# Kernel tuning notes

Hardware: AMD Instinct MI355X
Metric: run time of the kernel (lower is better)

## Reference

```python
import jax, jax.numpy as jnp
import numpy as np

B, L, D, H = 4, 2048, 1024, 16
DH = D // H


def setup_inputs() -> dict:
    key = jax.random.key(0)
    ks = jax.random.split(key, 8)
    scale = 1.0 / np.sqrt(D)
    q = jax.random.normal(ks[0], (B, L, D), dtype=jnp.float32)
    k = jax.random.normal(ks[1], (B, L, D), dtype=jnp.float32)
    v = jax.random.normal(ks[2], (B, L, D), dtype=jnp.float32)
    # causal mask: 1 = attend, 0 = masked (masked_fill(mask == 0, -inf))
    mask = jnp.tril(jnp.ones((L, L), dtype=bool))[None, None, :, :]
    mask = jnp.broadcast_to(mask, (B, 1, L, L))
    W_q = jax.random.normal(ks[3], (D, D), dtype=jnp.float32) * scale
    W_k = jax.random.normal(ks[4], (D, D), dtype=jnp.float32) * scale
    W_v = jax.random.normal(ks[5], (D, D), dtype=jnp.float32) * scale
    W_o = jax.random.normal(ks[6], (D, D), dtype=jnp.float32) * scale
    return {"q": q, "k": k, "v": v, "mask": mask,
            "W_q": W_q, "W_k": W_k, "W_v": W_v, "W_o": W_o}


def _split_heads(x):
    # [B, L, D] -> [B, H, L, DH]
    Bx, Lx, _ = x.shape
    return x.reshape(Bx, Lx, H, DH).transpose(0, 2, 1, 3)


def reference(q, k, v, mask, W_q, W_k, W_v, W_o):
    qh = _split_heads(q @ W_q.T)   # [B, H, L, DH]
    kh = _split_heads(k @ W_k.T)
    vh = _split_heads(v @ W_v.T)
    scores = jnp.einsum('bhqd,bhkd->bhqk', qh, kh) / np.sqrt(DH)
    scores = jnp.where(mask, scores, -jnp.inf)  # mask==0 -> -inf
    probs = jax.nn.softmax(scores, axis=-1)
    attn = jnp.einsum('bhqk,bhkd->bhqd', probs, vh)  # [B, H, L, DH]
    out = attn.transpose(0, 2, 1, 3).reshape(B, L, D)
    return out @ W_o.T
```

## Files before the change

kernel.cpp:

```cpp
#include <hip/hip_runtime.h>

typedef __attribute__((ext_vector_type(4))) float  f32x4;
typedef __attribute__((ext_vector_type(8))) short  s16x8;
typedef __attribute__((ext_vector_type(8))) unsigned short u16x8;
typedef __attribute__((ext_vector_type(4))) unsigned short u16x4;
typedef __attribute__((ext_vector_type(4))) unsigned int   u32x4;

static __device__ __forceinline__ unsigned short f2bf(float f) {
    unsigned int u = __builtin_bit_cast(unsigned int, f);
    u += 0x7fffu + ((u >> 16) & 1u);
    return (unsigned short)(u >> 16);
}

static __device__ __forceinline__ unsigned int cvt_pk_bf16(float lo, float hi) {
    unsigned int r;
    asm("v_cvt_pk_bf16_f32 %0, %1, %2" : "=v"(r) : "v"(lo), "v"(hi));
    return r;
}

static __device__ __forceinline__ void gload16(const void* g, void* l) {
    __builtin_amdgcn_global_load_lds(
        (const __attribute__((address_space(1))) void*)g,
        (__attribute__((address_space(3))) void*)l, 16, 0, 0);
}

template<int EPI>
__global__ __launch_bounds__(512)
void gemmF(const float* __restrict__ A0f, const float* __restrict__ A1f,
           const float* __restrict__ A2f, const unsigned short* __restrict__ Ab16,
           const float* __restrict__ B0f, const float* __restrict__ B1f,
           const float* __restrict__ B2f,
           unsigned short* __restrict__ O0, unsigned short* __restrict__ O1,
           unsigned short* __restrict__ O2, float* __restrict__ Of)
{
    __shared__ unsigned short Asw[2][256 * 64];
    __shared__ unsigned short Bsw[2][128 * 64];

    const int tid  = threadIdx.x;
    const int lane = tid & 63;
    const int wave = tid >> 6;
    const int wr   = wave >> 1, wc = wave & 1;
    const int g    = lane >> 4, l16 = lane & 15;

    const int nblk = (EPI == 0) ? 768 : 256;
    const int cpx  = nblk >> 3;
    const int wg   = (blockIdx.x & 7) * cpx + (blockIdx.x >> 3);
    const int bx   = wg & 7;
    const int byt  = wg >> 3;
    const int seg  = (EPI == 0) ? (byt >> 5) : 0;
    const int byl  = (EPI == 0) ? (byt & 31) : byt;

    const float* Arowf = nullptr;
    const unsigned short* Arowb = nullptr;
    if (EPI == 0) {
        const float* Af = seg == 0 ? A0f : seg == 1 ? A1f : A2f;
        Arowf = Af + (size_t)(byl * 256) * 1024;
    } else {
        Arowb = Ab16 + (size_t)(byl * 256) * 1024;
    }
    const float* Browf = (seg == 0 ? B0f : seg == 1 ? B1f : B2f)
                       + (size_t)(bx * 128) * 1024;

    f32x4 acc[4][4] = {};

    f32x4 alo[4], ahi[4];
    f32x4 blo[2], bhi[2];

    auto loadAf = [&](int kt2) {
        #pragma unroll
        for (int j = 0; j < 4; ++j) {
            const float* p = Arowf + (size_t)((j * 512 + tid) >> 3) * 1024
                           + kt2 * 64 + (tid & 7) * 8;
            alo[j] = *(const f32x4*)p;
            ahi[j] = *(const f32x4*)(p + 4);
        }
    };
    auto loadBf = [&](int kt2) {
        #pragma unroll
        for (int j = 0; j < 2; ++j) {
            const float* p = Browf + (size_t)((j * 512 + tid) >> 3) * 1024
                           + kt2 * 64 + (tid & 7) * 8;
            blo[j] = *(const f32x4*)p;
            bhi[j] = *(const f32x4*)(p + 4);
        }
    };
    auto writeA = [&](int buf) {
        #pragma unroll
        for (int j = 0; j < 4; ++j) {
            const int r = (j * 512 + tid) >> 3, c = tid & 7;
            u32x4 w;
            w[0] = cvt_pk_bf16(alo[j][0], alo[j][1]);
            w[1] = cvt_pk_bf16(alo[j][2], alo[j][3]);
            w[2] = cvt_pk_bf16(ahi[j][0], ahi[j][1]);
            w[3] = cvt_pk_bf16(ahi[j][2], ahi[j][3]);
            *(u32x4*)((char*)Asw[buf] + ((r * 128 + c * 16) ^ ((r & 7) << 4))) = w;
        }
    };
    auto writeB = [&](int buf) {
        #pragma unroll
        for (int j = 0; j < 2; ++j) {
            const int r = (j * 512 + tid) >> 3, c = tid & 7;
            u32x4 w;
            w[0] = cvt_pk_bf16(blo[j][0], blo[j][1]);
            w[1] = cvt_pk_bf16(blo[j][2], blo[j][3]);
            w[2] = cvt_pk_bf16(bhi[j][0], bhi[j][1]);
            w[3] = cvt_pk_bf16(bhi[j][2], bhi[j][3]);
            *(u32x4*)((char*)Bsw[buf] + ((r * 128 + c * 16) ^ ((r & 7) << 4))) = w;
        }
    };
    auto gloadA = [&](int buf, int kt2) {
        #pragma unroll
        for (int j = 0; j < 4; ++j) {
            const int r  = (j * 512 + tid) >> 3;
            const int cl = (tid & 7) ^ (r & 7);
            gload16(Arowb + (size_t)r * 1024 + kt2 * 64 + cl * 8,
                    (char*)Asw[buf] + j * 8192 + wave * 1024);
        }
    };
    auto lda = [&](const char* Ab, int mi, int ks) -> s16x8 {
        const int row = wr * 64 + mi * 16 + l16;
        const int off = (row * 128 + g * 16 + ks * 64) ^ ((row & 7) << 4);
        return __builtin_bit_cast(s16x8, *(const u16x8*)(Ab + off));
    };
    auto ldb = [&](const char* Bb, int ni, int ks) -> s16x8 {
        const int row = wc * 64 + ni * 16 + l16;
        const int off = (row * 128 + g * 16 + ks * 64) ^ ((row & 7) << 4);
        return __builtin_bit_cast(s16x8, *(const u16x8*)(Bb + off));
    };

    if (EPI == 0) { loadAf(0); } else { gloadA(0, 0); }
    loadBf(0);
    if (EPI == 0) writeA(0);
    writeB(0);
    __syncthreads();

    int cur = 0;
    for (int t = 0; t < 16; ++t) {
        const bool hn = (t + 1 < 16);
        if (hn) {
            if (EPI == 0) loadAf(t + 1); else gloadA(cur ^ 1, t + 1);
            loadBf(t + 1);
        }

        const char* Ab = (const char*)Asw[cur];
        const char* Bb = (const char*)Bsw[cur];
        #pragma unroll
        for (int ks = 0; ks < 2; ++ks) {
            s16x8 af[4], bf[4];
            #pragma unroll
            for (int mi = 0; mi < 4; ++mi) af[mi] = lda(Ab, mi, ks);
            #pragma unroll
            for (int ni = 0; ni < 4; ++ni) bf[ni] = ldb(Bb, ni, ks);
            __builtin_amdgcn_s_setprio(1);
            #pragma unroll
            for (int mi = 0; mi < 4; ++mi)
                #pragma unroll
                for (int ni = 0; ni < 4; ++ni)
                    acc[mi][ni] = __builtin_amdgcn_mfma_f32_16x16x32_bf16(
                        af[mi], bf[ni], acc[mi][ni], 0, 0, 0);
            __builtin_amdgcn_s_setprio(0);
        }

        if (hn) {
            if (EPI == 0) writeA(cur ^ 1);
            writeB(cur ^ 1);
        }
        __syncthreads();
        cur ^= 1;
    }

    #pragma unroll
    for (int mi = 0; mi < 4; ++mi) {
        #pragma unroll
        for (int ni = 0; ni < 4; ++ni) {
            const int gr0 = byl * 256 + wr * 64 + mi * 16 + g * 4;
            const int gc  = bx * 128 + wc * 64 + ni * 16 + l16;
            if (EPI == 0 && seg == 2) {
                const int b = gr0 >> 11, ll = gr0 & 2047;
                const int h = gc >> 6,  dh = gc & 63;
                u16x4 pk;
                #pragma unroll
                for (int rr = 0; rr < 4; ++rr) pk[rr] = f2bf(acc[mi][ni][rr]);
                *(u16x4*)(O2 + (size_t)((b * 16 + h) * 64 + dh) * 2048 + ll) = pk;
            } else {
                #pragma unroll
                for (int rr = 0; rr < 4; ++rr) {
                    const int gr = gr0 + rr;
                    float v = acc[mi][ni][rr];
                    if (EPI == 0) {
                        const int b = gr >> 11, ll = gr & 2047;
                        const int h = gc >> 6,  dh = gc & 63;
                        if (seg == 0) {
                            v *= 0.125f;
                            O0[(size_t)((b * 16 + h) * 2048 + ll) * 64 + dh] = f2bf(v);
                        } else {
                            O1[(size_t)((b * 16 + h) * 2048 + ll) * 64 + dh] = f2bf(v);
                        }
                    } else {
                        Of[(size_t)gr * 1024 + gc] = v;
                    }
                }
            }
        }
    }
}

__global__ __launch_bounds__(512)
void attn_kernel(const unsigned short* __restrict__ Qh,
                 const unsigned short* __restrict__ Kh,
                 const unsigned short* __restrict__ Vt,
                 unsigned short* __restrict__ Ctx)
{
    __shared__ unsigned short Ksw[2][64 * 64];
    __shared__ unsigned short Vsw[2][64 * 64];
    __shared__ unsigned short Psw[8][16 * 64];

    const int tid  = threadIdx.x;
    const int lane = tid & 63;
    const int wave = tid >> 6;
    const int g    = lane >> 4, l16 = lane & 15;
    const int qb   = 15 - (int)(blockIdx.x >> 6);
    const int bh   = blockIdx.x & 63;
    const int b    = bh >> 4, h = bh & 15;
    const int qrow0 = qb * 128 + wave * 16;
    const int ntile = 2 * qb + 2;

    const int sr = tid >> 3, sc = tid & 7;
    const int soff = (sr * 128 + sc * 16) ^ ((sr & 7) << 4);
    const unsigned short* kbase = Kh + ((size_t)bh * 2048 + sr) * 64 + sc * 8;
    const unsigned short* vbase = Vt + ((size_t)bh * 64 + sr) * 2048 + sc * 8;

    s16x8 qf[2];
    {
        const unsigned short* qp = Qh + ((size_t)bh * 2048 + qrow0 + l16) * 64 + g * 8;
        qf[0] = __builtin_bit_cast(s16x8, *(const u16x8*)qp);
        qf[1] = __builtin_bit_cast(s16x8, *(const u16x8*)(qp + 32));
    }

    f32x4 o[4] = {};
    float m = -3.0e38f, l = 0.f;

    *(u16x8*)((char*)Ksw[0] + soff) = *(const u16x8*)kbase;
    *(u16x8*)((char*)Vsw[0] + soff) = *(const u16x8*)vbase;
    __syncthreads();

    int cur = 0;
    for (int t = 0; t < ntile; ++t) {
        const int kv0 = t * 64;

        u16x8 kn, vn;
        const bool hn = (t + 1 < ntile);
        if (hn) {
            kn = *(const u16x8*)(kbase + (size_t)(kv0 + 64) * 64);
            vn = *(const u16x8*)(vbase + (kv0 + 64));
        }

        if (kv0 <= qrow0 + 15) {
            const char* Kb = (const char*)Ksw[cur];
            const char* Vb = (const char*)Vsw[cur];

            f32x4 st[4] = {};
            __builtin_amdgcn_s_setprio(1);
            #pragma unroll
            for (int nt = 0; nt < 4; ++nt) {
                #pragma unroll
                for (int ks = 0; ks < 2; ++ks) {
                    const int row = nt * 16 + l16;
                    const int off = (row * 128 + g * 16 + ks * 64) ^ ((row & 7) << 4);
                    s16x8 kf = __builtin_bit_cast(s16x8, *(const u16x8*)(Kb + off));
                    st[nt] = __builtin_amdgcn_mfma_f32_16x16x32_bf16(kf, qf[ks], st[nt], 0, 0, 0);
                }
            }
            __builtin_amdgcn_s_setprio(0);

            if (kv0 + 63 > qrow0) {
                const int q_g = qrow0 + l16;
                #pragma unroll
                for (int nt = 0; nt < 4; ++nt)
                    #pragma unroll
                    for (int rr = 0; rr < 4; ++rr) {
                        const int kv_g = kv0 + nt * 16 + g * 4 + rr;
                        if (kv_g > q_g) st[nt][rr] = -3.0e38f;
                    }
            }

            float pmax = fmaxf(
                fmaxf(fmaxf(fmaxf(st[0][0], st[0][1]), fmaxf(st[0][2], st[0][3])),
                      fmaxf(fmaxf(st[1][0], st[1][1]), fmaxf(st[1][2], st[1][3]))),
                fmaxf(fmaxf(fmaxf(st[2][0], st[2][1]), fmaxf(st[2][2], st[2][3])),
                      fmaxf(fmaxf(st[3][0], st[3][1]), fmaxf(st[3][2], st[3][3]))));
            pmax = fmaxf(pmax, __shfl_xor(pmax, 16));
            pmax = fmaxf(pmax, __shfl_xor(pmax, 32));

            if (__all(pmax <= m + 8.0f)) {
                float r0 = 0.f;
                #pragma unroll
                for (int nt = 0; nt < 4; ++nt)
                    #pragma unroll
                    for (int rr = 0; rr < 4; ++rr) {
                        const float p = __expf(st[nt][rr] - m);
                        st[nt][rr] = p;
                        r0 += p;
                    }
                r0 += __shfl_xor(r0, 16);
                r0 += __shfl_xor(r0, 32);
                l += r0;
            } else {
                const float mn = fmaxf(m, pmax);
                const float scf = __expf(m - mn);
                m = mn;
                float r0 = 0.f;
                #pragma unroll
                for (int nt = 0; nt < 4; ++nt)
                    #pragma unroll
                    for (int rr = 0; rr < 4; ++rr) {
                        const float p = __expf(st[nt][rr] - mn);
                        st[nt][rr] = p;
                        r0 += p;
                    }
                r0 += __shfl_xor(r0, 16);
                r0 += __shfl_xor(r0, 32);
                l = l * scf + r0;
                float sc4[4];
                #pragma unroll
                for (int rr = 0; rr < 4; ++rr) sc4[rr] = __shfl(scf, g * 4 + rr);
                #pragma unroll
                for (int nt = 0; nt < 4; ++nt)
                    #pragma unroll
                    for (int rr = 0; rr < 4; ++rr)
                        o[nt][rr] *= sc4[rr];
            }

            unsigned short* Pw = Psw[wave];
            #pragma unroll
            for (int nt = 0; nt < 4; ++nt) {
                const unsigned int w0 = cvt_pk_bf16(st[nt][0], st[nt][1]);
                const unsigned int w1 = cvt_pk_bf16(st[nt][2], st[nt][3]);
                const int off = (l16 * 128 + nt * 32 + g * 8) ^ ((l16 & 7) << 4);
                const unsigned long long dw = ((unsigned long long)w1 << 32) | w0;
                *(unsigned long long*)((char*)Pw + off) = dw;
            }

            __builtin_amdgcn_s_setprio(1);
            #pragma unroll
            for (int ks = 0; ks < 2; ++ks) {
                const int offp = (l16 * 128 + g * 16 + ks * 64) ^ ((l16 & 7) << 4);
                s16x8 pf = __builtin_bit_cast(s16x8, *(const u16x8*)((const char*)Pw + offp));
                #pragma unroll
                for (int nt = 0; nt < 4; ++nt) {
                    const int row = nt * 16 + l16;
                    const int off = (row * 128 + g * 16 + ks * 64) ^ ((row & 7) << 4);
                    s16x8 vf = __builtin_bit_cast(s16x8, *(const u16x8*)(Vb + off));
                    o[nt] = __builtin_amdgcn_mfma_f32_16x16x32_bf16(pf, vf, o[nt], 0, 0, 0);
                }
            }
            __builtin_amdgcn_s_setprio(0);
        }

        if (hn) {
            *(u16x8*)((char*)Ksw[cur ^ 1] + soff) = kn;
            *(u16x8*)((char*)Vsw[cur ^ 1] + soff) = vn;
        }
        __syncthreads();
        cur ^= 1;
    }

    #pragma unroll
    for (int rr = 0; rr < 4; ++rr) {
        const float lq = __shfl(l, g * 4 + rr);
        const float inv = 1.0f / lq;
        const int q_g = qrow0 + g * 4 + rr;
        #pragma unroll
        for (int nt = 0; nt < 4; ++nt) {
            const int d = nt * 16 + l16;
            Ctx[((size_t)b * 2048 + q_g) * 1024 + h * 64 + d] = f2bf(o[nt][rr] * inv);
        }
    }
}

extern "C" void kernel_launch(void* const* d_in, const int* in_sizes, int n_in,
                              void* d_out, int out_size, void* d_ws, size_t ws_size,
                              hipStream_t stream)
{
    const float* q  = (const float*)d_in[0];
    const float* k  = (const float*)d_in[1];
    const float* v  = (const float*)d_in[2];
    const float* Wq = (const float*)d_in[4];
    const float* Wk = (const float*)d_in[5];
    const float* Wv = (const float*)d_in[6];
    const float* Wo = (const float*)d_in[7];

    const size_t NE = (size_t)4 * 16 * 2048 * 64;
    unsigned short* Qh  = (unsigned short*)d_ws;
    unsigned short* Kh  = Qh + NE;
    unsigned short* Vt  = Kh + NE;
    unsigned short* Ctx = Vt + NE;
    float* outp = (float*)d_out;

    gemmF<0><<<dim3(768), dim3(512), 0, stream>>>(
        q, k, v, nullptr, Wq, Wk, Wv, Qh, Kh, Vt, nullptr);
    attn_kernel<<<dim3(1024), dim3(512), 0, stream>>>(Qh, Kh, Vt, Ctx);
    gemmF<1><<<dim3(256), dim3(512), 0, stream>>>(
        nullptr, nullptr, nullptr, Ctx, Wo, nullptr, nullptr,
        nullptr, nullptr, nullptr, outp);
}
```

Measured before the change: 179.0 us.

## Pre-convert weights to bf16 and use async LDS loads across GEMMs and attention

Adds a kernel that converts all four weight matrices to bf16 once per call, so the QKV GEMM can stream B through global_load_lds instead of loading fp32 and converting in registers. The output GEMM becomes a dedicated kernel with a three-stage async LDS pipeline gated by vmcnt waits. The attention kernel switches K/V staging from register round-trips to direct global-to-LDS loads. This adds an extra kernel launch and more workspace. The fallback path writes converted weights over the start of the workspace after attention, which looks like it overwrites Qh but is probably harmless because Qh is no longer read by then.

```diff
diff --git a/kernel.cpp b/kernel.cpp
--- a/kernel.cpp
+++ b/kernel.cpp
@@ -24,14 +24,31 @@
         (__attribute__((address_space(3))) void*)l, 16, 0, 0);
 }
 
-template<int EPI>
+__global__ __launch_bounds__(256)
+void convW_kernel(const float* __restrict__ wq, const float* __restrict__ wk,
+                  const float* __restrict__ wv, const float* __restrict__ wo,
+                  unsigned short* __restrict__ wb)
+{
+    const int wseg = blockIdx.x >> 9;
+    const float* src = wseg == 0 ? wq : wseg == 1 ? wk : wseg == 2 ? wv : wo;
+    unsigned short* dst = wb + (size_t)wseg * 1048576;
+    const size_t e0 = (size_t)(blockIdx.x & 511) * 2048 + threadIdx.x * 8;
+    f32x4 a = *(const f32x4*)(src + e0);
+    f32x4 b = *(const f32x4*)(src + e0 + 4);
+    u16x8 o;
+    #pragma unroll
+    for (int i = 0; i < 4; ++i) { o[i] = f2bf(a[i]); o[i + 4] = f2bf(b[i]); }
+    *(u16x8*)(dst + e0) = o;
+}
+
+template<int BSRC>
 __global__ __launch_bounds__(512)
-void gemmF(const float* __restrict__ A0f, const float* __restrict__ A1f,
-           const float* __restrict__ A2f, const unsigned short* __restrict__ Ab16,
-           const float* __restrict__ B0f, const float* __restrict__ B1f,
-           const float* __restrict__ B2f,
-           unsigned short* __restrict__ O0, unsigned short* __restrict__ O1,
-           unsigned short* __restrict__ O2, float* __restrict__ Of)
+void gemmQKV(const float* __restrict__ A0f, const float* __restrict__ A1f,
+             const float* __restrict__ A2f,
+             const float* __restrict__ B0f, const float* __restrict__ B1f,
+             const float* __restrict__ B2f, const unsigned short* __restrict__ Bb16,
+             unsigned short* __restrict__ O0, unsigned short* __restrict__ O1,
+             unsigned short* __restrict__ O2)
 {
     __shared__ unsigned short Asw[2][256 * 64];
     __shared__ unsigned short Bsw[2][128 * 64];
@@ -42,27 +59,20 @@
     const int wr   = wave >> 1, wc = wave & 1;
     const int g    = lane >> 4, l16 = lane & 15;
 
-    const int nblk = (EPI == 0) ? 768 : 256;
-    const int cpx  = nblk >> 3;
-    const int wg   = (blockIdx.x & 7) * cpx + (blockIdx.x >> 3);
+    const int wg   = (blockIdx.x & 7) * 96 + (blockIdx.x >> 3);
     const int bx   = wg & 7;
     const int byt  = wg >> 3;
-    const int seg  = (EPI == 0) ? (byt >> 5) : 0;
-    const int byl  = (EPI == 0) ? (byt & 31) : byt;
-
-    const float* Arowf = nullptr;
-    const unsigned short* Arowb = nullptr;
-    if (EPI == 0) {
-        const float* Af = seg == 0 ? A0f : seg == 1 ? A1f : A2f;
-        Arowf = Af + (size_t)(byl * 256) * 1024;
-    } else {
-        Arowb = Ab16 + (size_t)(byl * 256) * 1024;
-    }
+    const int seg  = byt >> 5;
+    const int byl  = byt & 31;
+
+    const float* Af = seg == 0 ? A0f : seg == 1 ? A1f : A2f;
+    const float* Arowf = Af + (size_t)(byl * 256) * 1024;
     const float* Browf = (seg == 0 ? B0f : seg == 1 ? B1f : B2f)
                        + (size_t)(bx * 128) * 1024;
+    const unsigned short* Browb = Bb16 + (size_t)seg * 1048576
+                                + (size_t)(bx * 128) * 1024;
 
     f32x4 acc[4][4] = {};
-
     f32x4 alo[4], ahi[4];
     f32x4 blo[2], bhi[2];
 
@@ -73,15 +83,6 @@
                            + kt2 * 64 + (tid & 7) * 8;
             alo[j] = *(const f32x4*)p;
             ahi[j] = *(const f32x4*)(p + 4);
-        }
-    };
-    auto loadBf = [&](int kt2) {
-        #pragma unroll
-        for (int j = 0; j < 2; ++j) {
-            const float* p = Browf + (size_t)((j * 512 + tid) >> 3) * 1024
-                           + kt2 * 64 + (tid & 7) * 8;
-            blo[j] = *(const f32x4*)p;
-            bhi[j] = *(const f32x4*)(p + 4);
         }
     };
     auto writeA = [&](int buf) {
@@ -96,6 +97,15 @@
             *(u32x4*)((char*)Asw[buf] + ((r * 128 + c * 16) ^ ((r & 7) << 4))) = w;
         }
     };
+    auto loadBf = [&](int kt2) {
+        #pragma unroll
+        for (int j = 0; j < 2; ++j) {
+            const float* p = Browf + (size_t)((j * 512 + tid) >> 3) * 1024
+                           + kt2 * 64 + (tid & 7) * 8;
+            blo[j] = *(const f32x4*)p;
+            bhi[j] = *(const f32x4*)(p + 4);
+        }
+    };
     auto writeB = [&](int buf) {
         #pragma unroll
         for (int j = 0; j < 2; ++j) {
@@ -108,13 +118,13 @@
             *(u32x4*)((char*)Bsw[buf] + ((r * 128 + c * 16) ^ ((r & 7) << 4))) = w;
         }
     };
-    auto gloadA = [&](int buf, int kt2) {
-        #pragma unroll
-        for (int j = 0; j < 4; ++j) {
+    auto gloadB = [&](int buf, int kt2) {
+        #pragma unroll
+        for (int j = 0; j < 2; ++j) {
             const int r  = (j * 512 + tid) >> 3;
             const int cl = (tid & 7) ^ (r & 7);
-            gload16(Arowb + (size_t)r * 1024 + kt2 * 64 + cl * 8,
-                    (char*)Asw[buf] + j * 8192 + wave * 1024);
+            gload16(Browb + (size_t)r * 1024 + kt2 * 64 + cl * 8,
+                    (char*)Bsw[buf] + j * 8192 + wave * 1024);
         }
     };
     auto lda = [&](const char* Ab, int mi, int ks) -> s16x8 {
@@ -128,18 +138,18 @@
         return __builtin_bit_cast(s16x8, *(const u16x8*)(Bb + off));
     };
 
-    if (EPI == 0) { loadAf(0); } else { gloadA(0, 0); }
-    loadBf(0);
-    if (EPI == 0) writeA(0);
-    writeB(0);
+    loadAf(0);
+    if (BSRC == 0) gloadB(0, 0); else loadBf(0);
+    writeA(0);
+    if (BSRC == 1) writeB(0);
     __syncthreads();
 
     int cur = 0;
     for (int t = 0; t < 16; ++t) {
         const bool hn = (t + 1 < 16);
         if (hn) {
-            if (EPI == 0) loadAf(t + 1); else gloadA(cur ^ 1, t + 1);
-            loadBf(t + 1);
+            loadAf(t + 1);
+            if (BSRC == 0) gloadB(cur ^ 1, t + 1); else loadBf(t + 1);
         }
 
         const char* Ab = (const char*)Asw[cur];
@@ -162,8 +172,8 @@
         }
 
         if (hn) {
-            if (EPI == 0) writeA(cur ^ 1);
-            writeB(cur ^ 1);
+            writeA(cur ^ 1);
+            if (BSRC == 1) writeB(cur ^ 1);
         }
         __syncthreads();
         cur ^= 1;
@@ -175,7 +185,7 @@
         for (int ni = 0; ni < 4; ++ni) {
             const int gr0 = byl * 256 + wr * 64 + mi * 16 + g * 4;
             const int gc  = bx * 128 + wc * 64 + ni * 16 + l16;
-            if (EPI == 0 && seg == 2) {
+            if (seg == 2) {
                 const int b = gr0 >> 11, ll = gr0 & 2047;
                 const int h = gc >> 6,  dh = gc & 63;
                 u16x4 pk;
@@ -187,20 +197,109 @@
                 for (int rr = 0; rr < 4; ++rr) {
                     const int gr = gr0 + rr;
                     float v = acc[mi][ni][rr];
-                    if (EPI == 0) {
-                        const int b = gr >> 11, ll = gr & 2047;
-                        const int h = gc >> 6,  dh = gc & 63;
-                        if (seg == 0) {
-                            v *= 0.125f;
-                            O0[(size_t)((b * 16 + h) * 2048 + ll) * 64 + dh] = f2bf(v);
-                        } else {
-                            O1[(size_t)((b * 16 + h) * 2048 + ll) * 64 + dh] = f2bf(v);
-                        }
+                    const int b = gr >> 11, ll = gr & 2047;
+                    const int h = gc >> 6,  dh = gc & 63;
+                    if (seg == 0) {
+                        v *= 0.125f;
+                        O0[(size_t)((b * 16 + h) * 2048 + ll) * 64 + dh] = f2bf(v);
                     } else {
-                        Of[(size_t)gr * 1024 + gc] = v;
+                        O1[(size_t)((b * 16 + h) * 2048 + ll) * 64 + dh] = f2bf(v);
                     }
                 }
             }
+        }
+    }
+}
+
+__global__ __launch_bounds__(512)
+void gemmOut(const unsigned short* __restrict__ A0,
+             const unsigned short* __restrict__ Bw,
+             float* __restrict__ Of)
+{
+    __shared__ unsigned short Asw[3][256 * 64];
+    __shared__ unsigned short Bsw[3][128 * 64];
+
+    const int tid  = threadIdx.x;
+    const int lane = tid & 63;
+    const int wave = tid >> 6;
+    const int wr   = wave >> 1, wc = wave & 1;
+    const int g    = lane >> 4, l16 = lane & 15;
+
+    const int wg   = (blockIdx.x & 7) * 32 + (blockIdx.x >> 3);
+    const int bx   = wg & 7;
+    const int byl  = wg >> 3;
+
+    const unsigned short* Arow = A0 + (size_t)(byl * 256) * 1024;
+    const unsigned short* Brow = Bw + (size_t)(bx * 128) * 1024;
+
+    f32x4 acc[4][4] = {};
+
+    auto stage = [&](int buf, int kt) {
+        #pragma unroll
+        for (int j = 0; j < 4; ++j) {
+            const int r  = (j * 512 + tid) >> 3;
+            const int cl = (tid & 7) ^ (r & 7);
+            gload16(Arow + (size_t)r * 1024 + kt * 64 + cl * 8,
+                    (char*)Asw[buf] + j * 8192 + wave * 1024);
+        }
+        #pragma unroll
+        for (int j = 0; j < 2; ++j) {
+            const int r  = (j * 512 + tid) >> 3;
+            const int cl = (tid & 7) ^ (r & 7);
+            gload16(Brow + (size_t)r * 1024 + kt * 64 + cl * 8,
+                    (char*)Bsw[buf] + j * 8192 + wave * 1024);
+        }
+    };
+
+    stage(0, 0);
+    stage(1, 1);
+    asm volatile("s_waitcnt vmcnt(6)" ::: "memory");
+    __builtin_amdgcn_s_barrier();
+
+    for (int kt = 0; kt < 16; ++kt) {
+        if (kt + 2 < 16) stage((kt + 2) % 3, kt + 2);
+
+        const char* Ab = (const char*)Asw[kt % 3];
+        const char* Bb = (const char*)Bsw[kt % 3];
+        #pragma unroll
+        for (int ks = 0; ks < 2; ++ks) {
+            s16x8 af[4], bf[4];
+            #pragma unroll
+            for (int mi = 0; mi < 4; ++mi) {
+                const int row = wr * 64 + mi * 16 + l16;
+                const int off = (row * 128 + g * 16 + ks * 64) ^ ((row & 7) << 4);
+                af[mi] = __builtin_bit_cast(s16x8, *(const u16x8*)(Ab + off));
+            }
+            #pragma unroll
+            for (int ni = 0; ni < 4; ++ni) {
+                const int row = wc * 64 + ni * 16 + l16;
+                const int off = (row * 128 + g * 16 + ks * 64) ^ ((row & 7) << 4);
+                bf[ni] = __builtin_bit_cast(s16x8, *(const u16x8*)(Bb + off));
+            }
+            __builtin_amdgcn_s_setprio(1);
+            #pragma unroll
+            for (int mi = 0; mi < 4; ++mi)
+                #pragma unroll
+                for (int ni = 0; ni < 4; ++ni)
+                    acc[mi][ni] = __builtin_amdgcn_mfma_f32_16x16x32_bf16(
+                        af[mi], bf[ni], acc[mi][ni], 0, 0, 0);
+            __builtin_amdgcn_s_setprio(0);
+        }
+
+        if (kt + 2 < 16) asm volatile("s_waitcnt vmcnt(6)" ::: "memory");
+        else             asm volatile("s_waitcnt vmcnt(0)" ::: "memory");
+        __builtin_amdgcn_s_barrier();
+    }
+
+    #pragma unroll
+    for (int mi = 0; mi < 4; ++mi) {
+        #pragma unroll
+        for (int ni = 0; ni < 4; ++ni) {
+            const int gr0 = byl * 256 + wr * 64 + mi * 16 + g * 4;
+            const int gc  = bx * 128 + wc * 64 + ni * 16 + l16;
+            #pragma unroll
+            for (int rr = 0; rr < 4; ++rr)
+                Of[(size_t)(gr0 + rr) * 1024 + gc] = acc[mi][ni][rr];
         }
     }
 }
@@ -225,10 +324,15 @@
     const int qrow0 = qb * 128 + wave * 16;
     const int ntile = 2 * qb + 2;
 
-    const int sr = tid >> 3, sc = tid & 7;
-    const int soff = (sr * 128 + sc * 16) ^ ((sr & 7) << 4);
-    const unsigned short* kbase = Kh + ((size_t)bh * 2048 + sr) * 64 + sc * 8;
-    const unsigned short* vbase = Vt + ((size_t)bh * 64 + sr) * 2048 + sc * 8;
+    const int sr = tid >> 3;
+    const int cl = (tid & 7) ^ (sr & 7);
+    const unsigned short* ksrc = Kh + ((size_t)bh * 2048 + sr) * 64 + cl * 8;
+    const unsigned short* vsrc = Vt + ((size_t)bh * 64 + sr) * 2048 + cl * 8;
+
+    auto stageKV = [&](int buf, int kv0) {
+        gload16(ksrc + (size_t)kv0 * 64, (char*)Ksw[buf] + wave * 1024);
+        gload16(vsrc + kv0,              (char*)Vsw[buf] + wave * 1024);
+    };
 
     s16x8 qf[2];
     {
@@ -240,20 +344,14 @@
     f32x4 o[4] = {};
     float m = -3.0e38f, l = 0.f;
 
-    *(u16x8*)((char*)Ksw[0] + soff) = *(const u16x8*)kbase;
-    *(u16x8*)((char*)Vsw[0] + soff) = *(const u16x8*)vbase;
+    stageKV(0, 0);
     __syncthreads();
 
     int cur = 0;
     for (int t = 0; t < ntile; ++t) {
         const int kv0 = t * 64;
-
-        u16x8 kn, vn;
         const bool hn = (t + 1 < ntile);
-        if (hn) {
-            kn = *(const u16x8*)(kbase + (size_t)(kv0 + 64) * 64);
-            vn = *(const u16x8*)(vbase + (kv0 + 64));
-        }
+        if (hn) stageKV(cur ^ 1, kv0 + 64);
 
         if (kv0 <= qrow0 + 15) {
             const char* Kb = (const char*)Ksw[cur];
@@ -357,10 +455,6 @@
             __builtin_amdgcn_s_setprio(0);
         }
 
-        if (hn) {
-            *(u16x8*)((char*)Ksw[cur ^ 1] + soff) = kn;
-            *(u16x8*)((char*)Vsw[cur ^ 1] + soff) = vn;
-        }
         __syncthreads();
         cur ^= 1;
     }
@@ -391,16 +485,27 @@
     const float* Wo = (const float*)d_in[7];
 
     const size_t NE = (size_t)4 * 16 * 2048 * 64;
+    const size_t WE = (size_t)1024 * 1024;
     unsigned short* Qh  = (unsigned short*)d_ws;
     unsigned short* Kh  = Qh + NE;
     unsigned short* Vt  = Kh + NE;
     unsigned short* Ctx = Vt + NE;
+    unsigned short* wb  = Ctx + NE;
     float* outp = (float*)d_out;
 
-    gemmF<0><<<dim3(768), dim3(512), 0, stream>>>(
-        q, k, v, nullptr, Wq, Wk, Wv, Qh, Kh, Vt, nullptr);
-    attn_kernel<<<dim3(1024), dim3(512), 0, stream>>>(Qh, Kh, Vt, Ctx);
-    gemmF<1><<<dim3(256), dim3(512), 0, stream>>>(
-        nullptr, nullptr, nullptr, Ctx, Wo, nullptr, nullptr,
-        nullptr, nullptr, nullptr, outp);
-}
+    if (ws_size >= 4 * NE * 2 + 4 * WE * 2) {
+        convW_kernel<<<dim3(2048), dim3(256), 0, stream>>>(Wq, Wk, Wv, Wo, wb);
+        gemmQKV<0><<<dim3(768), dim3(512), 0, stream>>>(
+            q, k, v, nullptr, nullptr, nullptr, wb, Qh, Kh, Vt);
+        attn_kernel<<<dim3(1024), dim3(512), 0, stream>>>(Qh, Kh, Vt, Ctx);
+        gemmOut<<<dim3(256), dim3(512), 0, stream>>>(Ctx, wb + 3 * WE, outp);
+    } else {
+        gemmQKV<1><<<dim3(768), dim3(512), 0, stream>>>(
+            q, k, v, Wq, Wk, Wv, nullptr, Qh, Kh, Vt);
+        attn_kernel<<<dim3(1024), dim3(512), 0, stream>>>(Qh, Kh, Vt, Ctx);
+        convW_kernel<<<dim3(2048), dim3(256), 0, stream>>>(Wq, Wk, Wv, Wo,
+                                                           (unsigned short*)d_ws);
+        gemmOut<<<dim3(256), dim3(512), 0, stream>>>(
+            Ctx, (unsigned short*)d_ws + 3 * WE, outp);
+    }
+}
```

New measurement: 195.2 us. 9.1% more time.
